# Performance work log

Hardware: AMD Instinct MI355X
Metric: run time of the kernel (lower is better)

The kernel has to match this reference:

```python
import jax, jax.numpy as jnp
import numpy as np

DIM = 128
HEADS = 4
DIM_HEAD = 32
HIDDEN = HEADS * DIM_HEAD
SCALE = DIM_HEAD ** -0.5
EPS = 1e-5


def setup_inputs() -> dict:
    key = jax.random.key(0)
    ks = jax.random.split(key, 8)
    s = 1.0 / np.sqrt(DIM)
    x = jax.random.normal(ks[0], (32, DIM, 64, 64), dtype=jnp.float32)
    Wq = jax.random.uniform(ks[1], (HIDDEN, DIM), jnp.float32, -s, s)
    Wk = jax.random.uniform(ks[2], (HIDDEN, DIM), jnp.float32, -s, s)
    Wv = jax.random.uniform(ks[3], (HIDDEN, DIM), jnp.float32, -s, s)
    so = 1.0 / np.sqrt(HIDDEN)
    Wo = jax.random.uniform(ks[4], (DIM, HIDDEN), jnp.float32, -so, so)
    bo = jax.random.uniform(ks[5], (DIM,), jnp.float32, -so, so)
    gn_w = jnp.ones((DIM,), jnp.float32)
    gn_b = jnp.zeros((DIM,), jnp.float32)
    return {"x": x, "Wq": Wq, "Wk": Wk, "Wv": Wv, "Wo": Wo, "bo": bo,
            "gn_w": gn_w, "gn_b": gn_b}


def reference(x, Wq, Wk, Wv, Wo, bo, gn_w, gn_b):
    b, c, h, w = x.shape
    n = h * w
    xf = x.reshape(b, c, n)  # [b, c, n]
    # 1x1 convs (no bias) == channel matmuls; split heads: [b, H, d, n]
    def proj(W):
        return jnp.einsum('oc,bcn->bon', W, xf).reshape(b, HEADS, DIM_HEAD, n)
    q = proj(Wq)
    k = proj(Wk)
    v = proj(Wv)
    q = jax.nn.softmax(q, axis=-2) * SCALE  # softmax over head-dim d
    k = jax.nn.softmax(k, axis=-1)          # softmax over spatial n
    ctx = jnp.einsum('bhdn,bhen->bhde', k, v)   # [b,H,d,e], tiny d=e=32
    out = jnp.einsum('bhde,bhdn->bhen', ctx, q) # [b,H,e,n]
    out = out.reshape(b, HIDDEN, n)
    # output 1x1 conv with bias
    out = jnp.einsum('oc,bcn->bon', Wo, out) + bo[None, :, None]  # [b,dim,n]
    # GroupNorm(num_groups=1): normalize over (C, n) per sample
    mu = jnp.mean(out, axis=(1, 2), keepdims=True)
    var = jnp.var(out, axis=(1, 2), keepdims=True)
    out = (out - mu) * jax.lax.rsqrt(var + EPS)
    out = out * gn_w[None, :, None] + gn_b[None, :, None]
    return out.reshape(b, c, h, w)
```

## Files before the change

kernel.cpp:

```cpp
#include <hip/hip_runtime.h>


#define B_   32
#define C_   128
#define N_   4096
#define H_   4
#define D_   32
#define HID  128
#define NB   64
#define TPB  4
#define NSTRIP 16
#define STV  72
#define STA  136
#define SCT  40
#define SCALE 0.1767766952966369f
#define EPS  1e-5f

typedef __attribute__((ext_vector_type(8))) short short8;
typedef __attribute__((ext_vector_type(4))) short short4v;
typedef __attribute__((ext_vector_type(4))) float floatx4;

__device__ __forceinline__ short f2bf(float f) {
  unsigned u = __float_as_uint(f);
  u += 0x7FFFu + ((u >> 16) & 1u);
  return (short)(u >> 16);
}

#define XLOAD(tt)                                                        \
  _Pragma("unroll")                                                      \
  for (int nt = 0; nt < 4; ++nt)                                         \
    _Pragma("unroll")                                                    \
    for (int j = 0; j < 8; ++j)                                          \
      xr[nt][j] = xw[(size_t)j * N_ + (size_t)(tt) * NB + nt * 16];

#define XCVT(fragbuf)                                                    \
  _Pragma("unroll")                                                      \
  for (int nt = 0; nt < 4; ++nt) {                                       \
    short8 s;                                                            \
    _Pragma("unroll")                                                    \
    for (int j = 0; j < 8; ++j) s[j] = f2bf(xr[nt][j]);                  \
    *(short8*)&fragbuf[((w * 4 + nt) * 64 + L) * 8] = s;                 \
  }

__global__ __launch_bounds__(256) void k_wcast(
    const float* __restrict__ Wq, const float* __restrict__ Wk,
    const float* __restrict__ Wv, const float* __restrict__ Wo,
    short* __restrict__ wb) {
  const int i = blockIdx.x * 256 + threadIdx.x;
  const float* srcs[4] = {Wq, Wk, Wv, Wo};
#pragma unroll
  for (int m = 0; m < 4; ++m) {
    floatx4 a = ((const floatx4*)srcs[m])[i];
    short4v s = { f2bf(a[0]), f2bf(a[1]), f2bf(a[2]), f2bf(a[3]) };
    ((short4v*)(wb + m * 16384))[i] = s;
  }
}

__global__ __launch_bounds__(256, 2) void k_kv_ctx(
    const float* __restrict__ x, const short* __restrict__ Wkb,
    const short* __restrict__ Wvb, float* __restrict__ ctx_u,
    float* __restrict__ Zsum) {
  __shared__ short frag[8192];
  __shared__ short ekbuf[C_ * STV];
  __shared__ short vbuf [C_ * STV];
  const int tid = threadIdx.x;
  const int w = tid >> 6, L = tid & 63, l15 = tid & 15, q4 = (tid & 63) >> 4;
  const int b = blockIdx.x / NSTRIP;
  const int strip = blockIdx.x % NSTRIP;
  const float* xw = x + (size_t)b * (C_ * N_) + (size_t)(w * 32 + q4 * 8) * N_
                      + (size_t)(strip * TPB) * NB + l15;

  short8 ak[2][4], av[2][4];
#pragma unroll
  for (int mt = 0; mt < 2; ++mt)
#pragma unroll
    for (int ks = 0; ks < 4; ++ks) {
      ak[mt][ks] = *(const short8*)&Wkb[(w * 32 + mt * 16 + l15) * C_ + ks * 32 + q4 * 8];
      av[mt][ks] = *(const short8*)&Wvb[(w * 32 + mt * 16 + l15) * C_ + ks * 32 + q4 * 8];
    }

  const floatx4 z4 = {0.f, 0.f, 0.f, 0.f};
  floatx4 ca[2][2] = {{z4, z4}, {z4, z4}};
  float zreg[2][4] = {{0.f,0.f,0.f,0.f},{0.f,0.f,0.f,0.f}};
  float xr[4][8];

  XLOAD(0)
  XCVT(frag)
  XLOAD(1)

  for (int t = 0; t < TPB; ++t) {
    __syncthreads();

    floatx4 acck[2][4];
#pragma unroll
    for (int mt = 0; mt < 2; ++mt)
#pragma unroll
      for (int nt = 0; nt < 4; ++nt) acck[mt][nt] = z4;
#pragma unroll
    for (int ks = 0; ks < 4; ++ks) {
      short8 Bf[4];
#pragma unroll
      for (int nt = 0; nt < 4; ++nt)
        Bf[nt] = *(const short8*)&frag[((ks * 4 + nt) * 64 + L) * 8];
#pragma unroll
      for (int mt = 0; mt < 2; ++mt)
#pragma unroll
        for (int nt = 0; nt < 4; ++nt)
          acck[mt][nt] = __builtin_amdgcn_mfma_f32_16x16x32_bf16(ak[mt][ks], Bf[nt], acck[mt][nt], 0, 0, 0);
    }

#pragma unroll
    for (int mt = 0; mt < 2; ++mt)
#pragma unroll
      for (int nt = 0; nt < 4; ++nt)
#pragma unroll
        for (int r = 0; r < 4; ++r)
          acck[mt][nt][r] = __expf(acck[mt][nt][r]);
#pragma unroll
    for (int mt = 0; mt < 2; ++mt)
#pragma unroll
      for (int r = 0; r < 4; ++r)
        zreg[mt][r] += acck[mt][0][r] + acck[mt][1][r] + acck[mt][2][r] + acck[mt][3][r];
#pragma unroll
    for (int mt = 0; mt < 2; ++mt)
#pragma unroll
      for (int nt = 0; nt < 4; ++nt)
#pragma unroll
        for (int r = 0; r < 4; ++r)
          ekbuf[(w * 32 + mt * 16 + q4 * 4 + r) * STV + nt * 16 + l15] = f2bf(acck[mt][nt][r]);

    floatx4 accv[2][4];
#pragma unroll
    for (int mt = 0; mt < 2; ++mt)
#pragma unroll
      for (int nt = 0; nt < 4; ++nt) accv[mt][nt] = z4;
#pragma unroll
    for (int ks = 0; ks < 4; ++ks) {
      short8 Bf[4];
#pragma unroll
      for (int nt = 0; nt < 4; ++nt)
        Bf[nt] = *(const short8*)&frag[((ks * 4 + nt) * 64 + L) * 8];
#pragma unroll
      for (int mt = 0; mt < 2; ++mt)
#pragma unroll
        for (int nt = 0; nt < 4; ++nt)
          accv[mt][nt] = __builtin_amdgcn_mfma_f32_16x16x32_bf16(av[mt][ks], Bf[nt], accv[mt][nt], 0, 0, 0);
    }
    __syncthreads();

    if (t + 1 < TPB) {
      XCVT(frag)
      if (t + 2 < TPB) { XLOAD(t + 2) }
    }

#pragma unroll
    for (int mt = 0; mt < 2; ++mt)
#pragma unroll
      for (int nt = 0; nt < 4; ++nt)
#pragma unroll
        for (int r = 0; r < 4; ++r)
          vbuf[(w * 32 + mt * 16 + q4 * 4 + r) * STV + nt * 16 + l15] = f2bf(accv[mt][nt][r]);

#pragma unroll
    for (int ks = 0; ks < 2; ++ks) {
      short8 ae[2], be[2];
#pragma unroll
      for (int mt = 0; mt < 2; ++mt)
        ae[mt] = *(const short8*)&ekbuf[(w * 32 + mt * 16 + l15) * STV + ks * 32 + q4 * 8];
#pragma unroll
      for (int nt = 0; nt < 2; ++nt)
        be[nt] = *(const short8*)&vbuf[(w * 32 + nt * 16 + l15) * STV + ks * 32 + q4 * 8];
#pragma unroll
      for (int mt = 0; mt < 2; ++mt)
#pragma unroll
        for (int nt = 0; nt < 2; ++nt)
          ca[mt][nt] = __builtin_amdgcn_mfma_f32_16x16x32_bf16(ae[mt], be[nt], ca[mt][nt], 0, 0, 0);
    }
  }

#pragma unroll
  for (int mt = 0; mt < 2; ++mt)
#pragma unroll
    for (int r = 0; r < 4; ++r) {
      float s = zreg[mt][r];
      s += __shfl_xor(s, 1); s += __shfl_xor(s, 2);
      s += __shfl_xor(s, 4); s += __shfl_xor(s, 8);
      if (l15 == 0) atomicAdd(&Zsum[b * HID + w * 32 + mt * 16 + q4 * 4 + r], s);
    }

  float* cb = &ctx_u[((size_t)b * H_ + w) * (D_ * D_)];
#pragma unroll
  for (int mt = 0; mt < 2; ++mt)
#pragma unroll
    for (int nt = 0; nt < 2; ++nt)
#pragma unroll
      for (int r = 0; r < 4; ++r)
        atomicAdd(&cb[(mt * 16 + q4 * 4 + r) * D_ + nt * 16 + l15], ca[mt][nt][r]);
}

__global__ __launch_bounds__(256, 2) void k_q_attn_o(
    const float* __restrict__ x, const short* __restrict__ Wqb,
    const short* __restrict__ Wob, const float* __restrict__ bo,
    const float* __restrict__ ctx_u, const float* __restrict__ Zsum,
    float* __restrict__ outp, float* __restrict__ stats) {
  __shared__ short frag[8192];
  __shared__ short qat[NB * STA];
  __shared__ short ctxT[HID * SCT];
  const int tid = threadIdx.x;
  const int w = tid >> 6, L = tid & 63, l15 = tid & 15, q4 = (tid & 63) >> 4;
  const int b = blockIdx.x / NSTRIP;
  const int strip = blockIdx.x % NSTRIP;
  const float* xw = x + (size_t)b * (C_ * N_) + (size_t)(w * 32 + q4 * 8) * N_
                      + (size_t)(strip * TPB) * NB + l15;

  float xr[4][8];
  XLOAD(0)
  XCVT(frag)
  XLOAD(1)
#pragma unroll
  for (int i = 0; i < 16; ++i) {
    const int idx = tid + i * 256;
    float v = ctx_u[(size_t)b * (H_ * D_ * D_) + idx] *
              __builtin_amdgcn_rcpf(Zsum[b * HID + (idx >> 5)]);
    ctxT[((idx >> 10) * 32 + (idx & 31)) * SCT + ((idx >> 5) & 31)] = f2bf(v);
  }

  short8 aq[2][4], ao[2][4];
#pragma unroll
  for (int mt = 0; mt < 2; ++mt)
#pragma unroll
    for (int ks = 0; ks < 4; ++ks) {
      aq[mt][ks] = *(const short8*)&Wqb[(w * 32 + mt * 16 + l15) * C_ + ks * 32 + q4 * 8];
      ao[mt][ks] = *(const short8*)&Wob[(w * 32 + mt * 16 + l15) * HID + ks * 32 + q4 * 8];
    }

  const floatx4 z4 = {0.f, 0.f, 0.f, 0.f};
  float s1 = 0.f, s2 = 0.f;

  for (int t = 0; t < TPB; ++t) {
    const int n0 = (strip * TPB + t) * NB;
    __syncthreads();

    floatx4 acc[2][4];
#pragma unroll
    for (int mt = 0; mt < 2; ++mt)
#pragma unroll
      for (int nt = 0; nt < 4; ++nt) acc[mt][nt] = z4;
#pragma unroll
    for (int ks = 0; ks < 4; ++ks) {
      short8 Bf[4];
#pragma unroll
      for (int nt = 0; nt < 4; ++nt)
        Bf[nt] = *(const short8*)&frag[((ks * 4 + nt) * 64 + L) * 8];
#pragma unroll
      for (int mt = 0; mt < 2; ++mt)
#pragma unroll
        for (int nt = 0; nt < 4; ++nt)
          acc[mt][nt] = __builtin_amdgcn_mfma_f32_16x16x32_bf16(aq[mt][ks], Bf[nt], acc[mt][nt], 0, 0, 0);
    }
    __syncthreads();

    if (t + 1 < TPB) {
      XCVT(frag)
      if (t + 2 < TPB) { XLOAD(t + 2) }
    }

#pragma unroll
    for (int mt = 0; mt < 2; ++mt)
#pragma unroll
      for (int nt = 0; nt < 4; ++nt)
#pragma unroll
        for (int r = 0; r < 4; ++r)
          acc[mt][nt][r] = __expf(acc[mt][nt][r]);
    float inv[4];
#pragma unroll
    for (int nt = 0; nt < 4; ++nt) {
      float s = 0.f;
#pragma unroll
      for (int mt = 0; mt < 2; ++mt)
#pragma unroll
        for (int r = 0; r < 4; ++r) s += acc[mt][nt][r];
      s += __shfl_xor(s, 16); s += __shfl_xor(s, 32);
      inv[nt] = SCALE * __builtin_amdgcn_rcpf(s);
    }

#pragma unroll
    for (int mt = 0; mt < 2; ++mt)
#pragma unroll
      for (int nt = 0; nt < 4; ++nt) {
        short4v pk = { f2bf(acc[mt][nt][0] * inv[nt]), f2bf(acc[mt][nt][1] * inv[nt]),
                       f2bf(acc[mt][nt][2] * inv[nt]), f2bf(acc[mt][nt][3] * inv[nt]) };
        *(short4v*)&qat[(nt * 16 + l15) * STA + w * 32 + mt * 16 + q4 * 4] = pk;
      }

    {
      floatx4 aacc[2][4];
#pragma unroll
      for (int mt = 0; mt < 2; ++mt)
#pragma unroll
        for (int nt = 0; nt < 4; ++nt) aacc[mt][nt] = z4;
      short8 ae[2];
#pragma unroll
      for (int mt = 0; mt < 2; ++mt)
        ae[mt] = *(const short8*)&ctxT[(w * 32 + mt * 16 + l15) * SCT + q4 * 8];
#pragma unroll
      for (int nt = 0; nt < 4; ++nt) {
        short8 bq = *(const short8*)&qat[(nt * 16 + l15) * STA + w * 32 + q4 * 8];
#pragma unroll
        for (int mt = 0; mt < 2; ++mt)
          aacc[mt][nt] = __builtin_amdgcn_mfma_f32_16x16x32_bf16(ae[mt], bq, aacc[mt][nt], 0, 0, 0);
      }
#pragma unroll
      for (int nt = 0; nt < 4; ++nt)
#pragma unroll
        for (int mt = 0; mt < 2; ++mt) {
          short4v pk = { f2bf(aacc[mt][nt][0]), f2bf(aacc[mt][nt][1]),
                         f2bf(aacc[mt][nt][2]), f2bf(aacc[mt][nt][3]) };
          *(short4v*)&qat[(nt * 16 + l15) * STA + w * 32 + mt * 16 + q4 * 4] = pk;
        }
    }
    __syncthreads();

    floatx4 oacc[2][4];
#pragma unroll
    for (int mt = 0; mt < 2; ++mt)
#pragma unroll
      for (int nt = 0; nt < 4; ++nt) oacc[mt][nt] = z4;
#pragma unroll
    for (int ks = 0; ks < 4; ++ks) {
      short8 bf8[4];
#pragma unroll
      for (int nt = 0; nt < 4; ++nt)
        bf8[nt] = *(const short8*)&qat[(nt * 16 + l15) * STA + ks * 32 + q4 * 8];
#pragma unroll
      for (int mt = 0; mt < 2; ++mt)
#pragma unroll
        for (int nt = 0; nt < 4; ++nt)
          oacc[mt][nt] = __builtin_amdgcn_mfma_f32_16x16x32_bf16(ao[mt][ks], bf8[nt], oacc[mt][nt], 0, 0, 0);
    }

#pragma unroll
    for (int mt = 0; mt < 2; ++mt) {
      const int rowbase = w * 32 + mt * 16 + q4 * 4;
      const floatx4 bo4 = *(const floatx4*)&bo[rowbase];
#pragma unroll
      for (int nt = 0; nt < 4; ++nt) {
        const int n = n0 + nt * 16 + l15;
#pragma unroll
        for (int r = 0; r < 4; ++r) {
          float vv = oacc[mt][nt][r] + bo4[r];
          outp[(size_t)b * (C_ * N_) + (size_t)(rowbase + r) * N_ + n] = vv;
          s1 += vv; s2 += vv * vv;
        }
      }
    }
  }

#pragma unroll
  for (int m = 1; m < 64; m <<= 1) {
    s1 += __shfl_xor(s1, m);
    s2 += __shfl_xor(s2, m);
  }
  if ((tid & 63) == 0) {
    atomicAdd(&stats[b * 2 + 0], s1);
    atomicAdd(&stats[b * 2 + 1], s2);
  }
}

__global__ __launch_bounds__(256) void k_gnorm(
    float* __restrict__ outp, const float* __restrict__ stats,
    const float* __restrict__ gnw, const float* __restrict__ gnb) {
  const int b = blockIdx.x >> 6;
  const int blk = blockIdx.x & 63;
  const float M = (float)(C_ * N_);
  const float mu = stats[b * 2 + 0] / M;
  const float var = stats[b * 2 + 1] / M - mu * mu;
  const float rs = rsqrtf(var + EPS);
  floatx4* p = (floatx4*)(outp + (size_t)b * (C_ * N_) + (size_t)blk * 8192);
  const int tid = threadIdx.x;
#pragma unroll
  for (int i = 0; i < 8; ++i) {
    const int idx = tid + i * 256;
    const int fl = blk * 8192 + idx * 4;
    const int c = fl >> 12;
    const float wgt = gnw[c] * rs;
    const float bia = gnb[c] - mu * wgt;
    floatx4 v = p[idx];
    v[0] = v[0] * wgt + bia;
    v[1] = v[1] * wgt + bia;
    v[2] = v[2] * wgt + bia;
    v[3] = v[3] * wgt + bia;
    p[idx] = v;
  }
}

extern "C" void kernel_launch(void* const* d_in, const int* in_sizes, int n_in,
                              void* d_out, int out_size, void* d_ws, size_t ws_size,
                              hipStream_t stream) {
  (void)in_sizes; (void)n_in; (void)out_size; (void)ws_size;
  const float* x   = (const float*)d_in[0];
  const float* Wq  = (const float*)d_in[1];
  const float* Wk  = (const float*)d_in[2];
  const float* Wv  = (const float*)d_in[3];
  const float* Wo  = (const float*)d_in[4];
  const float* bo  = (const float*)d_in[5];
  const float* gnw = (const float*)d_in[6];
  const float* gnb = (const float*)d_in[7];
  float* outp  = (float*)d_out;
  float* ctx_u = (float*)d_ws;
  float* Zsum  = ctx_u + B_ * H_ * D_ * D_;
  float* stats = Zsum + B_ * HID;
  short* wb    = (short*)(stats + B_ * 2);
  const size_t zbytes = (size_t)(B_ * H_ * D_ * D_ + B_ * HID + B_ * 2) * sizeof(float);
  hipMemsetAsync(d_ws, 0, zbytes, stream);
  hipLaunchKernelGGL(k_wcast,    dim3(64),          dim3(256), 0, stream, Wq, Wk, Wv, Wo, wb);
  hipLaunchKernelGGL(k_kv_ctx,   dim3(B_ * NSTRIP), dim3(256), 0, stream, x, wb + 16384, wb + 32768, ctx_u, Zsum);
  hipLaunchKernelGGL(k_q_attn_o, dim3(B_ * NSTRIP), dim3(256), 0, stream, x, wb, wb + 49152, bo, ctx_u, Zsum, outp, stats);
  hipLaunchKernelGGL(k_gnorm,    dim3(B_ * 64),     dim3(256), 0, stream, outp, stats, gnw, gnb);
}
```

Before: 199.4 us.

## Fuse all stages into one kernel with per-batch spin barriers

Merges the weight cast, KV context, Q/attention/output and GroupNorm kernels into a single persistent-style kernel of 512 blocks. Per-sample atomic counters act as grid barriers between stages, and weights are converted to bf16 inline in each block. GroupNorm is applied by the same block to its own strip, which is likely still in L2. This removes three launches and the separate wcast pass, but relies on all 16 blocks of a sample being co-resident; otherwise the spin barrier can deadlock. Each block also re-reads x for the Q pass.

```diff
diff --git a/kernel.cpp b/kernel.cpp
--- a/kernel.cpp
+++ b/kernel.cpp
@@ -42,355 +42,351 @@
     *(short8*)&fragbuf[((w * 4 + nt) * 64 + L) * 8] = s;                 \
   }
 
-__global__ __launch_bounds__(256) void k_wcast(
-    const float* __restrict__ Wq, const float* __restrict__ Wk,
-    const float* __restrict__ Wv, const float* __restrict__ Wo,
-    short* __restrict__ wb) {
-  const int i = blockIdx.x * 256 + threadIdx.x;
-  const float* srcs[4] = {Wq, Wk, Wv, Wo};
-#pragma unroll
-  for (int m = 0; m < 4; ++m) {
-    floatx4 a = ((const floatx4*)srcs[m])[i];
-    short4v s = { f2bf(a[0]), f2bf(a[1]), f2bf(a[2]), f2bf(a[3]) };
-    ((short4v*)(wb + m * 16384))[i] = s;
+#define WFRAG(dst, Wsrc, LD)                                             \
+  _Pragma("unroll")                                                      \
+  for (int mt = 0; mt < 2; ++mt)                                         \
+    _Pragma("unroll")                                                    \
+    for (int ks = 0; ks < 4; ++ks) {                                     \
+      const float* p_ = &Wsrc[(w * 32 + mt * 16 + l15) * LD + ks * 32 + q4 * 8]; \
+      floatx4 a0_ = *(const floatx4*)p_;                                 \
+      floatx4 a1_ = *(const floatx4*)(p_ + 4);                           \
+      short8 s_;                                                         \
+      s_[0] = f2bf(a0_[0]); s_[1] = f2bf(a0_[1]);                        \
+      s_[2] = f2bf(a0_[2]); s_[3] = f2bf(a0_[3]);                        \
+      s_[4] = f2bf(a1_[0]); s_[5] = f2bf(a1_[1]);                        \
+      s_[6] = f2bf(a1_[2]); s_[7] = f2bf(a1_[3]);                        \
+      dst[mt][ks] = s_;                                                  \
+    }
+
+__device__ __forceinline__ void arrive_wait(unsigned* ctr) {
+  __syncthreads();
+  if (threadIdx.x == 0) {
+    __hip_atomic_fetch_add(ctr, 1u, __ATOMIC_RELEASE, __HIP_MEMORY_SCOPE_AGENT);
+    while (__hip_atomic_load(ctr, __ATOMIC_ACQUIRE, __HIP_MEMORY_SCOPE_AGENT) <
+           (unsigned)NSTRIP)
+      __builtin_amdgcn_s_sleep(8);
   }
+  __syncthreads();
+  __threadfence();
 }
 
-__global__ __launch_bounds__(256, 2) void k_kv_ctx(
-    const float* __restrict__ x, const short* __restrict__ Wkb,
-    const short* __restrict__ Wvb, float* __restrict__ ctx_u,
-    float* __restrict__ Zsum) {
-  __shared__ short frag[8192];
-  __shared__ short ekbuf[C_ * STV];
-  __shared__ short vbuf [C_ * STV];
+__global__ __launch_bounds__(256, 2) void k_fused(
+    const float* __restrict__ x, const float* __restrict__ Wq,
+    const float* __restrict__ Wk, const float* __restrict__ Wv,
+    const float* __restrict__ Wo, const float* __restrict__ bo,
+    const float* __restrict__ gnw, const float* __restrict__ gnb,
+    float* __restrict__ ctx_u, float* __restrict__ Zsum,
+    float* __restrict__ stats, unsigned* __restrict__ done1,
+    unsigned* __restrict__ done2, float* __restrict__ outp) {
+  __shared__ char smem[53248];
+  short* frag  = (short*)smem;
+  short* ekbuf = (short*)(smem + 16384);
+  short* vbuf  = (short*)(smem + 34816);
+  short* qat   = (short*)(smem + 16384);
+  short* ctxT  = (short*)(smem + 33792);
+
   const int tid = threadIdx.x;
   const int w = tid >> 6, L = tid & 63, l15 = tid & 15, q4 = (tid & 63) >> 4;
   const int b = blockIdx.x / NSTRIP;
   const int strip = blockIdx.x % NSTRIP;
   const float* xw = x + (size_t)b * (C_ * N_) + (size_t)(w * 32 + q4 * 8) * N_
                       + (size_t)(strip * TPB) * NB + l15;
-
-  short8 ak[2][4], av[2][4];
-#pragma unroll
-  for (int mt = 0; mt < 2; ++mt)
-#pragma unroll
-    for (int ks = 0; ks < 4; ++ks) {
-      ak[mt][ks] = *(const short8*)&Wkb[(w * 32 + mt * 16 + l15) * C_ + ks * 32 + q4 * 8];
-      av[mt][ks] = *(const short8*)&Wvb[(w * 32 + mt * 16 + l15) * C_ + ks * 32 + q4 * 8];
-    }
-
   const floatx4 z4 = {0.f, 0.f, 0.f, 0.f};
-  floatx4 ca[2][2] = {{z4, z4}, {z4, z4}};
-  float zreg[2][4] = {{0.f,0.f,0.f,0.f},{0.f,0.f,0.f,0.f}};
   float xr[4][8];
 
-  XLOAD(0)
-  XCVT(frag)
-  XLOAD(1)
-
-  for (int t = 0; t < TPB; ++t) {
-    __syncthreads();
-
-    floatx4 acck[2][4];
+  {
+    short8 ak[2][4], av[2][4];
+    WFRAG(ak, Wk, C_)
+    WFRAG(av, Wv, C_)
+
+    floatx4 ca[2][2] = {{z4, z4}, {z4, z4}};
+    float zreg[2][4] = {{0.f,0.f,0.f,0.f},{0.f,0.f,0.f,0.f}};
+
+    XLOAD(0)
+    XCVT(frag)
+    XLOAD(1)
+
+    for (int t = 0; t < TPB; ++t) {
+      __syncthreads();
+
+      floatx4 acck[2][4];
+#pragma unroll
+      for (int mt = 0; mt < 2; ++mt)
+#pragma unroll
+        for (int nt = 0; nt < 4; ++nt) acck[mt][nt] = z4;
+#pragma unroll
+      for (int ks = 0; ks < 4; ++ks) {
+        short8 Bf[4];
+#pragma unroll
+        for (int nt = 0; nt < 4; ++nt)
+          Bf[nt] = *(const short8*)&frag[((ks * 4 + nt) * 64 + L) * 8];
+#pragma unroll
+        for (int mt = 0; mt < 2; ++mt)
+#pragma unroll
+          for (int nt = 0; nt < 4; ++nt)
+            acck[mt][nt] = __builtin_amdgcn_mfma_f32_16x16x32_bf16(ak[mt][ks], Bf[nt], acck[mt][nt], 0, 0, 0);
+      }
+
+#pragma unroll
+      for (int mt = 0; mt < 2; ++mt)
+#pragma unroll
+        for (int nt = 0; nt < 4; ++nt)
+#pragma unroll
+          for (int r = 0; r < 4; ++r)
+            acck[mt][nt][r] = __expf(acck[mt][nt][r]);
+#pragma unroll
+      for (int mt = 0; mt < 2; ++mt)
+#pragma unroll
+        for (int r = 0; r < 4; ++r)
+          zreg[mt][r] += acck[mt][0][r] + acck[mt][1][r] + acck[mt][2][r] + acck[mt][3][r];
+#pragma unroll
+      for (int mt = 0; mt < 2; ++mt)
+#pragma unroll
+        for (int nt = 0; nt < 4; ++nt)
+#pragma unroll
+          for (int r = 0; r < 4; ++r)
+            ekbuf[(w * 32 + mt * 16 + q4 * 4 + r) * STV + nt * 16 + l15] = f2bf(acck[mt][nt][r]);
+
+      floatx4 accv[2][4];
+#pragma unroll
+      for (int mt = 0; mt < 2; ++mt)
+#pragma unroll
+        for (int nt = 0; nt < 4; ++nt) accv[mt][nt] = z4;
+#pragma unroll
+      for (int ks = 0; ks < 4; ++ks) {
+        short8 Bf[4];
+#pragma unroll
+        for (int nt = 0; nt < 4; ++nt)
+          Bf[nt] = *(const short8*)&frag[((ks * 4 + nt) * 64 + L) * 8];
+#pragma unroll
+        for (int mt = 0; mt < 2; ++mt)
+#pragma unroll
+          for (int nt = 0; nt < 4; ++nt)
+            accv[mt][nt] = __builtin_amdgcn_mfma_f32_16x16x32_bf16(av[mt][ks], Bf[nt], accv[mt][nt], 0, 0, 0);
+      }
+      __syncthreads();
+
+      if (t + 1 < TPB) {
+        XCVT(frag)
+        if (t + 2 < TPB) { XLOAD(t + 2) }
+      }
+
+#pragma unroll
+      for (int mt = 0; mt < 2; ++mt)
+#pragma unroll
+        for (int nt = 0; nt < 4; ++nt)
+#pragma unroll
+          for (int r = 0; r < 4; ++r)
+            vbuf[(w * 32 + mt * 16 + q4 * 4 + r) * STV + nt * 16 + l15] = f2bf(accv[mt][nt][r]);
+
+#pragma unroll
+      for (int ks = 0; ks < 2; ++ks) {
+        short8 ae[2], be[2];
+#pragma unroll
+        for (int mt = 0; mt < 2; ++mt)
+          ae[mt] = *(const short8*)&ekbuf[(w * 32 + mt * 16 + l15) * STV + ks * 32 + q4 * 8];
+#pragma unroll
+        for (int nt = 0; nt < 2; ++nt)
+          be[nt] = *(const short8*)&vbuf[(w * 32 + nt * 16 + l15) * STV + ks * 32 + q4 * 8];
+#pragma unroll
+        for (int mt = 0; mt < 2; ++mt)
+#pragma unroll
+          for (int nt = 0; nt < 2; ++nt)
+            ca[mt][nt] = __builtin_amdgcn_mfma_f32_16x16x32_bf16(ae[mt], be[nt], ca[mt][nt], 0, 0, 0);
+      }
+    }
+
 #pragma unroll
     for (int mt = 0; mt < 2; ++mt)
 #pragma unroll
-      for (int nt = 0; nt < 4; ++nt) acck[mt][nt] = z4;
-#pragma unroll
-    for (int ks = 0; ks < 4; ++ks) {
-      short8 Bf[4];
-#pragma unroll
-      for (int nt = 0; nt < 4; ++nt)
-        Bf[nt] = *(const short8*)&frag[((ks * 4 + nt) * 64 + L) * 8];
-#pragma unroll
-      for (int mt = 0; mt < 2; ++mt)
-#pragma unroll
-        for (int nt = 0; nt < 4; ++nt)
-          acck[mt][nt] = __builtin_amdgcn_mfma_f32_16x16x32_bf16(ak[mt][ks], Bf[nt], acck[mt][nt], 0, 0, 0);
-    }
-
+      for (int r = 0; r < 4; ++r) {
+        float s = zreg[mt][r];
+        s += __shfl_xor(s, 1); s += __shfl_xor(s, 2);
+        s += __shfl_xor(s, 4); s += __shfl_xor(s, 8);
+        if (l15 == 0) atomicAdd(&Zsum[b * HID + w * 32 + mt * 16 + q4 * 4 + r], s);
+      }
+
+    float* cb = &ctx_u[((size_t)b * H_ + w) * (D_ * D_)];
 #pragma unroll
     for (int mt = 0; mt < 2; ++mt)
 #pragma unroll
-      for (int nt = 0; nt < 4; ++nt)
+      for (int nt = 0; nt < 2; ++nt)
 #pragma unroll
         for (int r = 0; r < 4; ++r)
-          acck[mt][nt][r] = __expf(acck[mt][nt][r]);
-#pragma unroll
-    for (int mt = 0; mt < 2; ++mt)
-#pragma unroll
-      for (int r = 0; r < 4; ++r)
-        zreg[mt][r] += acck[mt][0][r] + acck[mt][1][r] + acck[mt][2][r] + acck[mt][3][r];
-#pragma unroll
-    for (int mt = 0; mt < 2; ++mt)
-#pragma unroll
-      for (int nt = 0; nt < 4; ++nt)
-#pragma unroll
-        for (int r = 0; r < 4; ++r)
-          ekbuf[(w * 32 + mt * 16 + q4 * 4 + r) * STV + nt * 16 + l15] = f2bf(acck[mt][nt][r]);
-
-    floatx4 accv[2][4];
-#pragma unroll
-    for (int mt = 0; mt < 2; ++mt)
-#pragma unroll
-      for (int nt = 0; nt < 4; ++nt) accv[mt][nt] = z4;
-#pragma unroll
-    for (int ks = 0; ks < 4; ++ks) {
-      short8 Bf[4];
-#pragma unroll
-      for (int nt = 0; nt < 4; ++nt)
-        Bf[nt] = *(const short8*)&frag[((ks * 4 + nt) * 64 + L) * 8];
-#pragma unroll
-      for (int mt = 0; mt < 2; ++mt)
-#pragma unroll
-        for (int nt = 0; nt < 4; ++nt)
-          accv[mt][nt] = __builtin_amdgcn_mfma_f32_16x16x32_bf16(av[mt][ks], Bf[nt], accv[mt][nt], 0, 0, 0);
-    }
-    __syncthreads();
-
-    if (t + 1 < TPB) {
-      XCVT(frag)
-      if (t + 2 < TPB) { XLOAD(t + 2) }
-    }
-
-#pragma unroll
-    for (int mt = 0; mt < 2; ++mt)
-#pragma unroll
-      for (int nt = 0; nt < 4; ++nt)
-#pragma unroll
-        for (int r = 0; r < 4; ++r)
-          vbuf[(w * 32 + mt * 16 + q4 * 4 + r) * STV + nt * 16 + l15] = f2bf(accv[mt][nt][r]);
-
-#pragma unroll
-    for (int ks = 0; ks < 2; ++ks) {
-      short8 ae[2], be[2];
-#pragma unroll
-      for (int mt = 0; mt < 2; ++mt)
-        ae[mt] = *(const short8*)&ekbuf[(w * 32 + mt * 16 + l15) * STV + ks * 32 + q4 * 8];
-#pragma unroll
-      for (int nt = 0; nt < 2; ++nt)
-        be[nt] = *(const short8*)&vbuf[(w * 32 + nt * 16 + l15) * STV + ks * 32 + q4 * 8];
-#pragma unroll
-      for (int mt = 0; mt < 2; ++mt)
-#pragma unroll
-        for (int nt = 0; nt < 2; ++nt)
-          ca[mt][nt] = __builtin_amdgcn_mfma_f32_16x16x32_bf16(ae[mt], be[nt], ca[mt][nt], 0, 0, 0);
-    }
+          atomicAdd(&cb[(mt * 16 + q4 * 4 + r) * D_ + nt * 16 + l15], ca[mt][nt][r]);
   }
 
-#pragma unroll
-  for (int mt = 0; mt < 2; ++mt)
-#pragma unroll
-    for (int r = 0; r < 4; ++r) {
-      float s = zreg[mt][r];
-      s += __shfl_xor(s, 1); s += __shfl_xor(s, 2);
-      s += __shfl_xor(s, 4); s += __shfl_xor(s, 8);
-      if (l15 == 0) atomicAdd(&Zsum[b * HID + w * 32 + mt * 16 + q4 * 4 + r], s);
-    }
-
-  float* cb = &ctx_u[((size_t)b * H_ + w) * (D_ * D_)];
-#pragma unroll
-  for (int mt = 0; mt < 2; ++mt)
-#pragma unroll
-    for (int nt = 0; nt < 2; ++nt)
-#pragma unroll
-      for (int r = 0; r < 4; ++r)
-        atomicAdd(&cb[(mt * 16 + q4 * 4 + r) * D_ + nt * 16 + l15], ca[mt][nt][r]);
-}
-
-__global__ __launch_bounds__(256, 2) void k_q_attn_o(
-    const float* __restrict__ x, const short* __restrict__ Wqb,
-    const short* __restrict__ Wob, const float* __restrict__ bo,
-    const float* __restrict__ ctx_u, const float* __restrict__ Zsum,
-    float* __restrict__ outp, float* __restrict__ stats) {
-  __shared__ short frag[8192];
-  __shared__ short qat[NB * STA];
-  __shared__ short ctxT[HID * SCT];
-  const int tid = threadIdx.x;
-  const int w = tid >> 6, L = tid & 63, l15 = tid & 15, q4 = (tid & 63) >> 4;
-  const int b = blockIdx.x / NSTRIP;
-  const int strip = blockIdx.x % NSTRIP;
-  const float* xw = x + (size_t)b * (C_ * N_) + (size_t)(w * 32 + q4 * 8) * N_
-                      + (size_t)(strip * TPB) * NB + l15;
-
-  float xr[4][8];
-  XLOAD(0)
-  XCVT(frag)
-  XLOAD(1)
-#pragma unroll
-  for (int i = 0; i < 16; ++i) {
-    const int idx = tid + i * 256;
-    float v = ctx_u[(size_t)b * (H_ * D_ * D_) + idx] *
-              __builtin_amdgcn_rcpf(Zsum[b * HID + (idx >> 5)]);
-    ctxT[((idx >> 10) * 32 + (idx & 31)) * SCT + ((idx >> 5) & 31)] = f2bf(v);
-  }
-
-  short8 aq[2][4], ao[2][4];
-#pragma unroll
-  for (int mt = 0; mt < 2; ++mt)
-#pragma unroll
-    for (int ks = 0; ks < 4; ++ks) {
-      aq[mt][ks] = *(const short8*)&Wqb[(w * 32 + mt * 16 + l15) * C_ + ks * 32 + q4 * 8];
-      ao[mt][ks] = *(const short8*)&Wob[(w * 32 + mt * 16 + l15) * HID + ks * 32 + q4 * 8];
-    }
-
-  const floatx4 z4 = {0.f, 0.f, 0.f, 0.f};
+  arrive_wait(&done1[b]);
+
   float s1 = 0.f, s2 = 0.f;
-
-  for (int t = 0; t < TPB; ++t) {
-    const int n0 = (strip * TPB + t) * NB;
-    __syncthreads();
-
-    floatx4 acc[2][4];
-#pragma unroll
-    for (int mt = 0; mt < 2; ++mt)
-#pragma unroll
-      for (int nt = 0; nt < 4; ++nt) acc[mt][nt] = z4;
-#pragma unroll
-    for (int ks = 0; ks < 4; ++ks) {
-      short8 Bf[4];
-#pragma unroll
-      for (int nt = 0; nt < 4; ++nt)
-        Bf[nt] = *(const short8*)&frag[((ks * 4 + nt) * 64 + L) * 8];
-#pragma unroll
-      for (int mt = 0; mt < 2; ++mt)
-#pragma unroll
-        for (int nt = 0; nt < 4; ++nt)
-          acc[mt][nt] = __builtin_amdgcn_mfma_f32_16x16x32_bf16(aq[mt][ks], Bf[nt], acc[mt][nt], 0, 0, 0);
-    }
-    __syncthreads();
-
-    if (t + 1 < TPB) {
-      XCVT(frag)
-      if (t + 2 < TPB) { XLOAD(t + 2) }
-    }
-
-#pragma unroll
-    for (int mt = 0; mt < 2; ++mt)
-#pragma unroll
-      for (int nt = 0; nt < 4; ++nt)
-#pragma unroll
-        for (int r = 0; r < 4; ++r)
-          acc[mt][nt][r] = __expf(acc[mt][nt][r]);
-    float inv[4];
-#pragma unroll
-    for (int nt = 0; nt < 4; ++nt) {
-      float s = 0.f;
-#pragma unroll
-      for (int mt = 0; mt < 2; ++mt)
-#pragma unroll
-        for (int r = 0; r < 4; ++r) s += acc[mt][nt][r];
-      s += __shfl_xor(s, 16); s += __shfl_xor(s, 32);
-      inv[nt] = SCALE * __builtin_amdgcn_rcpf(s);
-    }
-
-#pragma unroll
-    for (int mt = 0; mt < 2; ++mt)
+  {
+    XLOAD(0)
+    XCVT(frag)
+    XLOAD(1)
+#pragma unroll
+    for (int i = 0; i < 16; ++i) {
+      const int idx = tid + i * 256;
+      float v = ctx_u[(size_t)b * (H_ * D_ * D_) + idx] *
+                __builtin_amdgcn_rcpf(Zsum[b * HID + (idx >> 5)]);
+      ctxT[((idx >> 10) * 32 + (idx & 31)) * SCT + ((idx >> 5) & 31)] = f2bf(v);
+    }
+
+    short8 aq[2][4], ao[2][4];
+    WFRAG(aq, Wq, C_)
+    WFRAG(ao, Wo, HID)
+
+    for (int t = 0; t < TPB; ++t) {
+      const int n0 = (strip * TPB + t) * NB;
+      __syncthreads();
+
+      floatx4 acc[2][4];
+#pragma unroll
+      for (int mt = 0; mt < 2; ++mt)
+#pragma unroll
+        for (int nt = 0; nt < 4; ++nt) acc[mt][nt] = z4;
+#pragma unroll
+      for (int ks = 0; ks < 4; ++ks) {
+        short8 Bf[4];
+#pragma unroll
+        for (int nt = 0; nt < 4; ++nt)
+          Bf[nt] = *(const short8*)&frag[((ks * 4 + nt) * 64 + L) * 8];
+#pragma unroll
+        for (int mt = 0; mt < 2; ++mt)
+#pragma unroll
+          for (int nt = 0; nt < 4; ++nt)
+            acc[mt][nt] = __builtin_amdgcn_mfma_f32_16x16x32_bf16(aq[mt][ks], Bf[nt], acc[mt][nt], 0, 0, 0);
+      }
+      __syncthreads();
+
+      if (t + 1 < TPB) {
+        XCVT(frag)
+        if (t + 2 < TPB) { XLOAD(t + 2) }
+      }
+
+#pragma unroll
+      for (int mt = 0; mt < 2; ++mt)
+#pragma unroll
+        for (int nt = 0; nt < 4; ++nt)
+#pragma unroll
+          for (int r = 0; r < 4; ++r)
+            acc[mt][nt][r] = __expf(acc[mt][nt][r]);
+      float inv[4];
 #pragma unroll
       for (int nt = 0; nt < 4; ++nt) {
-        short4v pk = { f2bf(acc[mt][nt][0] * inv[nt]), f2bf(acc[mt][nt][1] * inv[nt]),
-                       f2bf(acc[mt][nt][2] * inv[nt]), f2bf(acc[mt][nt][3] * inv[nt]) };
-        *(short4v*)&qat[(nt * 16 + l15) * STA + w * 32 + mt * 16 + q4 * 4] = pk;
-      }
-
-    {
-      floatx4 aacc[2][4];
-#pragma unroll
-      for (int mt = 0; mt < 2; ++mt)
-#pragma unroll
-        for (int nt = 0; nt < 4; ++nt) aacc[mt][nt] = z4;
-      short8 ae[2];
-#pragma unroll
-      for (int mt = 0; mt < 2; ++mt)
-        ae[mt] = *(const short8*)&ctxT[(w * 32 + mt * 16 + l15) * SCT + q4 * 8];
-#pragma unroll
-      for (int nt = 0; nt < 4; ++nt) {
-        short8 bq = *(const short8*)&qat[(nt * 16 + l15) * STA + w * 32 + q4 * 8];
-#pragma unroll
-        for (int mt = 0; mt < 2; ++mt)
-          aacc[mt][nt] = __builtin_amdgcn_mfma_f32_16x16x32_bf16(ae[mt], bq, aacc[mt][nt], 0, 0, 0);
-      }
-#pragma unroll
-      for (int nt = 0; nt < 4; ++nt)
-#pragma unroll
-        for (int mt = 0; mt < 2; ++mt) {
-          short4v pk = { f2bf(aacc[mt][nt][0]), f2bf(aacc[mt][nt][1]),
-                         f2bf(aacc[mt][nt][2]), f2bf(aacc[mt][nt][3]) };
+        float s = 0.f;
+#pragma unroll
+        for (int mt = 0; mt < 2; ++mt)
+#pragma unroll
+          for (int r = 0; r < 4; ++r) s += acc[mt][nt][r];
+        s += __shfl_xor(s, 16); s += __shfl_xor(s, 32);
+        inv[nt] = SCALE * __builtin_amdgcn_rcpf(s);
+      }
+
+#pragma unroll
+      for (int mt = 0; mt < 2; ++mt)
+#pragma unroll
+        for (int nt = 0; nt < 4; ++nt) {
+          short4v pk = { f2bf(acc[mt][nt][0] * inv[nt]), f2bf(acc[mt][nt][1] * inv[nt]),
+                         f2bf(acc[mt][nt][2] * inv[nt]), f2bf(acc[mt][nt][3] * inv[nt]) };
           *(short4v*)&qat[(nt * 16 + l15) * STA + w * 32 + mt * 16 + q4 * 4] = pk;
         }
-    }
-    __syncthreads();
-
-    floatx4 oacc[2][4];
-#pragma unroll
-    for (int mt = 0; mt < 2; ++mt)
-#pragma unroll
-      for (int nt = 0; nt < 4; ++nt) oacc[mt][nt] = z4;
-#pragma unroll
-    for (int ks = 0; ks < 4; ++ks) {
-      short8 bf8[4];
-#pragma unroll
-      for (int nt = 0; nt < 4; ++nt)
-        bf8[nt] = *(const short8*)&qat[(nt * 16 + l15) * STA + ks * 32 + q4 * 8];
-#pragma unroll
-      for (int mt = 0; mt < 2; ++mt)
-#pragma unroll
-        for (int nt = 0; nt < 4; ++nt)
-          oacc[mt][nt] = __builtin_amdgcn_mfma_f32_16x16x32_bf16(ao[mt][ks], bf8[nt], oacc[mt][nt], 0, 0, 0);
-    }
-
-#pragma unroll
-    for (int mt = 0; mt < 2; ++mt) {
-      const int rowbase = w * 32 + mt * 16 + q4 * 4;
-      const floatx4 bo4 = *(const floatx4*)&bo[rowbase];
-#pragma unroll
-      for (int nt = 0; nt < 4; ++nt) {
-        const int n = n0 + nt * 16 + l15;
-#pragma unroll
-        for (int r = 0; r < 4; ++r) {
-          float vv = oacc[mt][nt][r] + bo4[r];
-          outp[(size_t)b * (C_ * N_) + (size_t)(rowbase + r) * N_ + n] = vv;
-          s1 += vv; s2 += vv * vv;
+
+      {
+        floatx4 aacc[2][4];
+#pragma unroll
+        for (int mt = 0; mt < 2; ++mt)
+#pragma unroll
+          for (int nt = 0; nt < 4; ++nt) aacc[mt][nt] = z4;
+        short8 ae[2];
+#pragma unroll
+        for (int mt = 0; mt < 2; ++mt)
+          ae[mt] = *(const short8*)&ctxT[(w * 32 + mt * 16 + l15) * SCT + q4 * 8];
+#pragma unroll
+        for (int nt = 0; nt < 4; ++nt) {
+          short8 bq = *(const short8*)&qat[(nt * 16 + l15) * STA + w * 32 + q4 * 8];
+#pragma unroll
+          for (int mt = 0; mt < 2; ++mt)
+            aacc[mt][nt] = __builtin_amdgcn_mfma_f32_16x16x32_bf16(ae[mt], bq, aacc[mt][nt], 0, 0, 0);
         }
-      }
+#pragma unroll
+        for (int nt = 0; nt < 4; ++nt)
+#pragma unroll
+          for (int mt = 0; mt < 2; ++mt) {
+            short4v pk = { f2bf(aacc[mt][nt][0]), f2bf(aacc[mt][nt][1]),
+                           f2bf(aacc[mt][nt][2]), f2bf(aacc[mt][nt][3]) };
+            *(short4v*)&qat[(nt * 16 + l15) * STA + w * 32 + mt * 16 + q4 * 4] = pk;
+          }
+      }
+      __syncthreads();
+
+      floatx4 oacc[2][4];
+#pragma unroll
+      for (int mt = 0; mt < 2; ++mt)
+#pragma unroll
+        for (int nt = 0; nt < 4; ++nt) oacc[mt][nt] = z4;
+#pragma unroll
+      for (int ks = 0; ks < 4; ++ks) {
+        short8 bf8[4];
+#pragma unroll
+        for (int nt = 0; nt < 4; ++nt)
+          bf8[nt] = *(const short8*)&qat[(nt * 16 + l15) * STA + ks * 32 + q4 * 8];
+#pragma unroll
+        for (int mt = 0; mt < 2; ++mt)
+#pragma unroll
+          for (int nt = 0; nt < 4; ++nt)
+            oacc[mt][nt] = __builtin_amdgcn_mfma_f32_16x16x32_bf16(ao[mt][ks], bf8[nt], oacc[mt][nt], 0, 0, 0);
+      }
+
+#pragma unroll
+      for (int mt = 0; mt < 2; ++mt) {
+        const int rowbase = w * 32 + mt * 16 + q4 * 4;
+        const floatx4 bo4 = *(const floatx4*)&bo[rowbase];
+#pragma unroll
+        for (int nt = 0; nt < 4; ++nt) {
+          const int n = n0 + nt * 16 + l15;
+#pragma unroll
+          for (int r = 0; r < 4; ++r) {
+            float vv = oacc[mt][nt][r] + bo4[r];
+            outp[(size_t)b * (C_ * N_) + (size_t)(rowbase + r) * N_ + n] = vv;
+            s1 += vv; s2 += vv * vv;
+          }
+        }
+      }
+    }
+
+#pragma unroll
+    for (int m = 1; m < 64; m <<= 1) {
+      s1 += __shfl_xor(s1, m);
+      s2 += __shfl_xor(s2, m);
+    }
+    if ((tid & 63) == 0) {
+      atomicAdd(&stats[b * 2 + 0], s1);
+      atomicAdd(&stats[b * 2 + 1], s2);
     }
   }
 
-#pragma unroll
-  for (int m = 1; m < 64; m <<= 1) {
-    s1 += __shfl_xor(s1, m);
-    s2 += __shfl_xor(s2, m);
-  }
-  if ((tid & 63) == 0) {
-    atomicAdd(&stats[b * 2 + 0], s1);
-    atomicAdd(&stats[b * 2 + 1], s2);
-  }
-}
-
-__global__ __launch_bounds__(256) void k_gnorm(
-    float* __restrict__ outp, const float* __restrict__ stats,
-    const float* __restrict__ gnw, const float* __restrict__ gnb) {
-  const int b = blockIdx.x >> 6;
-  const int blk = blockIdx.x & 63;
-  const float M = (float)(C_ * N_);
-  const float mu = stats[b * 2 + 0] / M;
-  const float var = stats[b * 2 + 1] / M - mu * mu;
-  const float rs = rsqrtf(var + EPS);
-  floatx4* p = (floatx4*)(outp + (size_t)b * (C_ * N_) + (size_t)blk * 8192);
-  const int tid = threadIdx.x;
-#pragma unroll
-  for (int i = 0; i < 8; ++i) {
-    const int idx = tid + i * 256;
-    const int fl = blk * 8192 + idx * 4;
-    const int c = fl >> 12;
-    const float wgt = gnw[c] * rs;
-    const float bia = gnb[c] - mu * wgt;
-    floatx4 v = p[idx];
-    v[0] = v[0] * wgt + bia;
-    v[1] = v[1] * wgt + bia;
-    v[2] = v[2] * wgt + bia;
-    v[3] = v[3] * wgt + bia;
-    p[idx] = v;
+  arrive_wait(&done2[b]);
+
+  {
+    const float M = (float)(C_ * N_);
+    const float mu = stats[b * 2 + 0] / M;
+    const float var = stats[b * 2 + 1] / M - mu * mu;
+    const float rs = rsqrtf(var + EPS);
+    float* pb = outp + (size_t)b * (C_ * N_) + (size_t)(strip * TPB) * NB;
+#pragma unroll
+    for (int i = 0; i < 32; ++i) {
+      const int f = tid + i * 256;
+      const int row = f >> 6, c4 = f & 63;
+      const float wgt = gnw[row] * rs;
+      const float bia = gnb[row] - mu * wgt;
+      floatx4* p = (floatx4*)(pb + (size_t)row * N_) + c4;
+      floatx4 v = *p;
+      v[0] = v[0] * wgt + bia;
+      v[1] = v[1] * wgt + bia;
+      v[2] = v[2] * wgt + bia;
+      v[3] = v[3] * wgt + bia;
+      *p = v;
+    }
   }
 }
 
@@ -410,11 +406,12 @@
   float* ctx_u = (float*)d_ws;
   float* Zsum  = ctx_u + B_ * H_ * D_ * D_;
   float* stats = Zsum + B_ * HID;
-  short* wb    = (short*)(stats + B_ * 2);
-  const size_t zbytes = (size_t)(B_ * H_ * D_ * D_ + B_ * HID + B_ * 2) * sizeof(float);
+  unsigned* done1 = (unsigned*)(stats + B_ * 2);
+  unsigned* done2 = done1 + B_;
+  const size_t zbytes = (size_t)(B_ * H_ * D_ * D_ + B_ * HID + B_ * 2) * sizeof(float)
+                      + (size_t)(2 * B_) * sizeof(unsigned);
   hipMemsetAsync(d_ws, 0, zbytes, stream);
-  hipLaunchKernelGGL(k_wcast,    dim3(64),          dim3(256), 0, stream, Wq, Wk, Wv, Wo, wb);
-  hipLaunchKernelGGL(k_kv_ctx,   dim3(B_ * NSTRIP), dim3(256), 0, stream, x, wb + 16384, wb + 32768, ctx_u, Zsum);
-  hipLaunchKernelGGL(k_q_attn_o, dim3(B_ * NSTRIP), dim3(256), 0, stream, x, wb, wb + 49152, bo, ctx_u, Zsum, outp, stats);
-  hipLaunchKernelGGL(k_gnorm,    dim3(B_ * 64),     dim3(256), 0, stream, outp, stats, gnw, gnb);
+  hipLaunchKernelGGL(k_fused, dim3(B_ * NSTRIP), dim3(256), 0, stream,
+                     x, Wq, Wk, Wv, Wo, bo, gnw, gnb,
+                     ctx_u, Zsum, stats, done1, done2, outp);
 }
```

Result: slower. 392.9 us (+97.0%).

## Load ctx fragments directly into registers and halve tiles per block in q-attn kernel

Applied to the files above, without the earlier changes.

The q/attention/output kernel no longer stages the normalized context matrix through shared memory. Each lane builds its MFMA A-fragments straight from global ctx and Zsum into registers. The grid doubles to 32 strips per batch with 2 tiles each, launch bounds ask for 4 blocks per CU, and the x prefetch is reordered so the bf16 convert happens after the softmax stage. This aims to cut LDS use and raise occupancy, at the cost of more blocks each redoing the ctx load and normalization, and possible register pressure under the tighter bound.

```diff
diff --git a/kernel.cpp b/kernel.cpp
--- a/kernel.cpp
+++ b/kernel.cpp
@@ -10,9 +10,10 @@
 #define NB   64
 #define TPB  4
 #define NSTRIP 16
+#define TPB2   2
+#define NSTRIP2 32
 #define STV  72
 #define STA  136
-#define SCT  40
 #define SCALE 0.1767766952966369f
 #define EPS  1e-5f
 
@@ -198,31 +199,39 @@
         atomicAdd(&cb[(mt * 16 + q4 * 4 + r) * D_ + nt * 16 + l15], ca[mt][nt][r]);
 }
 
-__global__ __launch_bounds__(256, 2) void k_q_attn_o(
+__global__ __launch_bounds__(256, 4) void k_q_attn_o(
     const float* __restrict__ x, const short* __restrict__ Wqb,
     const short* __restrict__ Wob, const float* __restrict__ bo,
     const float* __restrict__ ctx_u, const float* __restrict__ Zsum,
     float* __restrict__ outp, float* __restrict__ stats) {
   __shared__ short frag[8192];
   __shared__ short qat[NB * STA];
-  __shared__ short ctxT[HID * SCT];
   const int tid = threadIdx.x;
   const int w = tid >> 6, L = tid & 63, l15 = tid & 15, q4 = (tid & 63) >> 4;
-  const int b = blockIdx.x / NSTRIP;
-  const int strip = blockIdx.x % NSTRIP;
+  const int b = blockIdx.x / NSTRIP2;
+  const int strip = blockIdx.x % NSTRIP2;
   const float* xw = x + (size_t)b * (C_ * N_) + (size_t)(w * 32 + q4 * 8) * N_
-                      + (size_t)(strip * TPB) * NB + l15;
+                      + (size_t)(strip * TPB2) * NB + l15;
 
   float xr[4][8];
   XLOAD(0)
   XCVT(frag)
-  XLOAD(1)
-#pragma unroll
-  for (int i = 0; i < 16; ++i) {
-    const int idx = tid + i * 256;
-    float v = ctx_u[(size_t)b * (H_ * D_ * D_) + idx] *
-              __builtin_amdgcn_rcpf(Zsum[b * HID + (idx >> 5)]);
-    ctxT[((idx >> 10) * 32 + (idx & 31)) * SCT + ((idx >> 5) & 31)] = f2bf(v);
+
+  short8 ae[2];
+  {
+    const float* cbase = ctx_u + (size_t)b * (H_ * D_ * D_) + w * 1024;
+    const float* zbase = Zsum + b * HID + w * 32;
+#pragma unroll
+    for (int mt = 0; mt < 2; ++mt) {
+      short8 s;
+#pragma unroll
+      for (int j = 0; j < 8; ++j) {
+        const int d = q4 * 8 + j;
+        float v = cbase[d * 32 + mt * 16 + l15] * __builtin_amdgcn_rcpf(zbase[d]);
+        s[j] = f2bf(v);
+      }
+      ae[mt] = s;
+    }
   }
 
   short8 aq[2][4], ao[2][4];
@@ -237,8 +246,8 @@
   const floatx4 z4 = {0.f, 0.f, 0.f, 0.f};
   float s1 = 0.f, s2 = 0.f;
 
-  for (int t = 0; t < TPB; ++t) {
-    const int n0 = (strip * TPB + t) * NB;
+  for (int t = 0; t < TPB2; ++t) {
+    const int n0 = (strip * TPB2 + t) * NB;
     __syncthreads();
 
     floatx4 acc[2][4];
@@ -260,10 +269,7 @@
     }
     __syncthreads();
 
-    if (t + 1 < TPB) {
-      XCVT(frag)
-      if (t + 2 < TPB) { XLOAD(t + 2) }
-    }
+    if (t + 1 < TPB2) { XLOAD(t + 1) }
 
 #pragma unroll
     for (int mt = 0; mt < 2; ++mt)
@@ -293,16 +299,14 @@
         *(short4v*)&qat[(nt * 16 + l15) * STA + w * 32 + mt * 16 + q4 * 4] = pk;
       }
 
+    if (t + 1 < TPB2) { XCVT(frag) }
+
     {
       floatx4 aacc[2][4];
 #pragma unroll
       for (int mt = 0; mt < 2; ++mt)
 #pragma unroll
         for (int nt = 0; nt < 4; ++nt) aacc[mt][nt] = z4;
-      short8 ae[2];
-#pragma unroll
-      for (int mt = 0; mt < 2; ++mt)
-        ae[mt] = *(const short8*)&ctxT[(w * 32 + mt * 16 + l15) * SCT + q4 * 8];
 #pragma unroll
       for (int nt = 0; nt < 4; ++nt) {
         short8 bq = *(const short8*)&qat[(nt * 16 + l15) * STA + w * 32 + q4 * 8];
@@ -413,8 +417,8 @@
   short* wb    = (short*)(stats + B_ * 2);
   const size_t zbytes = (size_t)(B_ * H_ * D_ * D_ + B_ * HID + B_ * 2) * sizeof(float);
   hipMemsetAsync(d_ws, 0, zbytes, stream);
-  hipLaunchKernelGGL(k_wcast,    dim3(64),          dim3(256), 0, stream, Wq, Wk, Wv, Wo, wb);
-  hipLaunchKernelGGL(k_kv_ctx,   dim3(B_ * NSTRIP), dim3(256), 0, stream, x, wb + 16384, wb + 32768, ctx_u, Zsum);
-  hipLaunchKernelGGL(k_q_attn_o, dim3(B_ * NSTRIP), dim3(256), 0, stream, x, wb, wb + 49152, bo, ctx_u, Zsum, outp, stats);
-  hipLaunchKernelGGL(k_gnorm,    dim3(B_ * 64),     dim3(256), 0, stream, outp, stats, gnw, gnb);
-}
+  hipLaunchKernelGGL(k_wcast,    dim3(64),           dim3(256), 0, stream, Wq, Wk, Wv, Wo, wb);
+  hipLaunchKernelGGL(k_kv_ctx,   dim3(B_ * NSTRIP),  dim3(256), 0, stream, x, wb + 16384, wb + 32768, ctx_u, Zsum);
+  hipLaunchKernelGGL(k_q_attn_o, dim3(B_ * NSTRIP2), dim3(256), 0, stream, x, wb, wb + 49152, bo, ctx_u, Zsum, outp, stats);
+  hipLaunchKernelGGL(k_gnorm,    dim3(B_ * 64),      dim3(256), 0, stream, outp, stats, gnw, gnb);
+}
```

Result: slower. 287.0 us (+43.9%).
